# Kernel optimization log

Measured on AMD Instinct MI355X. Metric: run time of the kernel, lower is better.

## Reference

```python
import jax, jax.numpy as jnp
import numpy as np

K = 3          # kernel_size
STRIDE = 1
PAD = 1
DIL = 1


def conv2d(x, w, b, stride=STRIDE, pad=PAD, dil=DIL):
    y = jax.lax.conv_general_dilated(
        x, w, window_strides=(stride, stride),
        padding=((pad, pad), (pad, pad)), rhs_dilation=(dil, dil),
        dimension_numbers=('NCHW', 'OIHW', 'NCHW'))
    if b is not None:
        y = y + b[None, :, None, None]
    return y


def bilinear_gather(x, py, px):
    """Zero-padded bilinear sampling.
    x: [B,C,H,W]; py,px: [B,K2,Ho,Wo] float coords. Returns [B,C,K2,Ho,Wo].
    Matches torchvision deform_conv2d: out-of-range corners contribute zero."""
    B, C, H, W = x.shape
    y0 = jnp.floor(py)
    x0 = jnp.floor(px)
    wy1 = py - y0
    wx1 = px - x0
    wy0 = 1.0 - wy1
    wx0 = 1.0 - wx1
    xf = x.reshape(B, C, H * W)

    def corner(yi, xi, wgt):
        valid = (yi >= 0) & (yi < H) & (xi >= 0) & (xi < W)
        yc = jnp.clip(yi, 0, H - 1).astype(jnp.int32)
        xc = jnp.clip(xi, 0, W - 1).astype(jnp.int32)
        idx = (yc * W + xc).reshape(B, 1, -1)            # [B,1,K2*Ho*Wo]
        v = jnp.take_along_axis(xf, idx, axis=2)         # [B,C,K2*Ho*Wo]
        v = v.reshape(B, C, *yi.shape[1:])               # [B,C,K2,Ho,Wo]
        w = (wgt * valid.astype(x.dtype))[:, None]       # [B,1,K2,Ho,Wo]
        return v * w

    return (corner(y0, x0, wy0 * wx0) + corner(y0, x0 + 1, wy0 * wx1)
            + corner(y0 + 1, x0, wy1 * wx0) + corner(y0 + 1, x0 + 1, wy1 * wx1))


def reference(x, w_offset, b_offset, w_mask, b_mask, w_deform):
    B, C, H, W = x.shape
    K2 = K * K
    offset = conv2d(x, w_offset, b_offset)               # [B,2*K2,Ho,Wo]
    mask = jax.nn.sigmoid(conv2d(x, w_mask, b_mask))     # [B,K2,Ho,Wo]
    Ho, Wo = offset.shape[2], offset.shape[3]

    off = offset.reshape(B, K2, 2, Ho, Wo)
    dy, dx = off[:, :, 0], off[:, :, 1]                  # [B,K2,Ho,Wo]

    ky = (jnp.arange(K2) // K).astype(x.dtype) * DIL     # kernel tap row offsets
    kx = (jnp.arange(K2) % K).astype(x.dtype) * DIL
    base_y = (jnp.arange(Ho) * STRIDE - PAD).astype(x.dtype)
    base_x = (jnp.arange(Wo) * STRIDE - PAD).astype(x.dtype)
    py = dy + base_y[None, None, :, None] + ky[None, :, None, None]
    px = dx + base_x[None, None, None, :] + kx[None, :, None, None]

    val = bilinear_gather(x, py, px)                     # [B,C,K2,Ho,Wo]
    val = val * mask[:, None]                            # modulation

    w = w_deform.reshape(w_deform.shape[0], C, K2)       # [Cout,Cin,K2]
    return jnp.einsum('bckhw,ock->bohw', val, w)


def setup_inputs() -> dict:
    key = jax.random.key(0)
    k = jax.random.split(key, 6)
    B, Cin, Cout, H, W = 2, 64, 64, 224, 224
    x = jax.random.normal(k[0], (B, Cin, H, W), dtype=jnp.float32)
    # source zero-inits offset/mask convs; use small random weights to exercise
    # fractional, scattered sampling coordinates.
    w_offset = jax.random.normal(k[1], (2 * K * K, Cin, K, K), dtype=jnp.float32) * 0.01
    b_offset = jnp.zeros((2 * K * K,), dtype=jnp.float32)
    w_mask = jax.random.normal(k[2], (K * K, Cin, K, K), dtype=jnp.float32) * 0.01
    b_mask = jnp.zeros((K * K,), dtype=jnp.float32)
    w_deform = jax.random.normal(k[3], (Cout, Cin, K, K), dtype=jnp.float32) * (1.0 / np.sqrt(Cin * K * K))
    return {"x": x, "w_offset": w_offset, "b_offset": b_offset,
            "w_mask": w_mask, "b_mask": b_mask, "w_deform": w_deform}
```

## Files before the change

kernel.cpp:

```cpp
#include <hip/hip_runtime.h>
#include <hip/hip_bf16.h>
#include <math.h>

constexpr int B    = 2;
constexpr int C    = 64;
constexpr int H    = 224;
constexpr int W    = 224;
constexpr int Hp   = 226;
constexpr int Wp   = 226;
constexpr int OCO  = 18;
constexpr int OM   = 27;
constexpr int COUT = 64;
constexpr int HW   = H * W;
constexpr int NPIX = B * HW;
constexpr int CK   = C * 9;
constexpr int CPB  = 32;

constexpr int PAD_BLKS = (HW / 32) * B;
constexpr int BOR_N    = B * 900 * 8;
constexpr int BOR_BLKS = (BOR_N + 255) / 256;
constexpr int WA_BLKS  = (COUT * CK) / 256;
constexpr int WOM_BLKS = (32 * CK) / 256;

typedef short  bf16x8 __attribute__((ext_vector_type(8)));
typedef float  f32x4  __attribute__((ext_vector_type(4)));

__device__ inline unsigned short f2bf(float f) {
    union { float f; unsigned u; } v; v.f = f;
    unsigned r = v.u + 0x7FFF + ((v.u >> 16) & 1);
    return (unsigned short)(r >> 16);
}
__device__ inline unsigned cvtpk(float a, float b) {
    __hip_bfloat162 h = __float22bfloat162_rn(make_float2(a, b));
    union { __hip_bfloat162 h; unsigned u; } cv; cv.h = h;
    return cv.u;
}
__device__ inline float blo(unsigned u) { union { unsigned u; float f; } c; c.u = u << 16; return c.f; }
__device__ inline float bhi(unsigned u) { union { unsigned u; float f; } c; c.u = u & 0xFFFF0000u; return c.f; }

__global__ __launch_bounds__(256) void k_prep(const float* __restrict__ x,
                                              unsigned short* __restrict__ xp,
                                              const float* __restrict__ wd,
                                              unsigned short* __restrict__ wA,
                                              const float* __restrict__ w_off,
                                              const float* __restrict__ w_msk,
                                              const float* __restrict__ b_off,
                                              const float* __restrict__ b_msk,
                                              unsigned short* __restrict__ womA,
                                              float* __restrict__ biasv) {
    __shared__ float tile[64][33];
    const int bx  = blockIdx.x;
    const int tid = threadIdx.x;

    if (bx < PAD_BLKS) {
        const int b   = bx / (HW / 32);
        const int hw0 = (bx % (HW / 32)) * 32;
        const float* xb = x + (size_t)b * C * HW;
        {
            const int c  = tid >> 2;
            const int hq = (tid & 3) * 8;
            const float* src = xb + (size_t)c * HW + hw0 + hq;
            const float4 a0 = *reinterpret_cast<const float4*>(src);
            const float4 a1 = *reinterpret_cast<const float4*>(src + 4);
            tile[c][hq + 0] = a0.x; tile[c][hq + 1] = a0.y;
            tile[c][hq + 2] = a0.z; tile[c][hq + 3] = a0.w;
            tile[c][hq + 4] = a1.x; tile[c][hq + 5] = a1.y;
            tile[c][hq + 6] = a1.z; tile[c][hq + 7] = a1.w;
        }
        __syncthreads();
        unsigned short* xpb = xp + (size_t)b * Hp * Wp * C;
        const int l15 = tid & 15, hh = tid >> 4;
        const int c = l15 * 4;
#pragma unroll
        for (int half = 0; half < 2; ++half) {
            int hw = hw0 + half * 16 + hh;
            int y = hw / W, xx = hw % W;
            float t0 = tile[c][half * 16 + hh],     t1 = tile[c + 1][half * 16 + hh];
            float t2 = tile[c + 2][half * 16 + hh], t3 = tile[c + 3][half * 16 + hh];
            *reinterpret_cast<uint2*>(xpb + ((size_t)(y + 1) * Wp + (xx + 1)) * C + c) =
                make_uint2(cvtpk(t0, t1), cvtpk(t2, t3));
        }
        return;
    }
    if (bx < PAD_BLKS + BOR_BLKS) {
        int i = (bx - PAD_BLKS) * 256 + tid;
        if (i >= BOR_N) return;
        int chunk = i & 7;
        int cell  = (i >> 3) % 900;
        int b     = (i >> 3) / 900;
        int y, xx;
        if      (cell < 226) { y = 0;              xx = cell; }
        else if (cell < 452) { y = Hp - 1;         xx = cell - 226; }
        else if (cell < 676) { y = cell - 452 + 1; xx = 0; }
        else                 { y = cell - 676 + 1; xx = Wp - 1; }
        uint4 z = make_uint4(0u, 0u, 0u, 0u);
        *reinterpret_cast<uint4*>(xp + ((size_t)b * Hp * Wp + y * Wp + xx) * C + chunk * 8) = z;
        return;
    }
    if (bx < PAD_BLKS + BOR_BLKS + WA_BLKS) {
        int i  = (bx - PAD_BLKS - BOR_BLKS) * 256 + tid;
        int o  = i / CK;
        int kc = i % CK;
        int k  = kc >> 6;
        int c  = kc & 63;
        wA[i] = f2bf(wd[((size_t)o * C + c) * 9 + k]);
        return;
    }
    {
        int i = (bx - PAD_BLKS - BOR_BLKS - WA_BLKS) * 256 + tid;
        if (i < 32) biasv[i] = (i < OCO) ? b_off[i] : (i < OM) ? b_msk[i - OCO] : 0.f;
        int oc = i / CK;
        int kc = i % CK;
        int k  = kc >> 6;
        int c  = kc & 63;
        float v = (oc < OCO) ? w_off[((size_t)oc * C + c) * 9 + k]
                : (oc < OM)  ? w_msk[((size_t)(oc - OCO) * C + c) * 9 + k]
                             : 0.f;
        womA[i] = f2bf(v);
    }
}

__global__ __launch_bounds__(256, 4) void k_fused(const unsigned short* __restrict__ xp,
                                                  const unsigned short* __restrict__ womA,
                                                  const unsigned short* __restrict__ wA,
                                                  const float* __restrict__ biasv,
                                                  float* __restrict__ out) {
    __shared__ __align__(16) unsigned short imcol[CPB * CK];
    __shared__ float som[CPB][28];
    const int tid  = threadIdx.x;
    const int lane = tid & 63;
    const int wv   = tid >> 6;
    const int q    = lane >> 4;
    const int l15  = lane & 15;
    int bid = blockIdx.x;
    bid = (bid & 7) * (gridDim.x >> 3) + (bid >> 3);
    const int pix0 = bid * CPB;
    const int bb   = pix0 / HW;
    const unsigned short* xb = xp + (size_t)bb * Hp * Wp * C;

    const int c0 = l15 * 4;

#pragma unroll
    for (int pi = 0; pi < 2; ++pi) {
        const int p_local = pi * 16 + wv * 4 + q;
        const int pix = pix0 + p_local;
        const int hw  = pix - bb * HW;
        const int y   = hw / W;
        const int xx  = hw % W;
        int wbase = p_local * (CK * 2) + l15 * 8;
        wbase ^= (p_local & 7) << 4;
#pragma unroll
        for (int k = 0; k < 9; ++k) {
            const int ky = k / 3, kx = k % 3;
            const uint2 v = *reinterpret_cast<const uint2*>(
                xb + ((size_t)(y + ky) * Wp + (xx + kx)) * C + c0);
            *reinterpret_cast<uint2*>(reinterpret_cast<char*>(imcol) + wbase + k * 128) = v;
        }
    }
    __syncthreads();

    {
        f32x4 acc = {0.f, 0.f, 0.f, 0.f};
        const int m = wv & 1, n = wv >> 1;
        const unsigned short* a0 = womA + (size_t)(m * 16 + l15) * CK;
        const int row = n * 16 + l15;
#pragma unroll 3
        for (int ks = 0; ks < 18; ++ks) {
            int byte = row * (CK * 2) + ks * 64 + q * 16;
            byte ^= (row & 7) << 4;
            const bf16x8 bfv = *reinterpret_cast<const bf16x8*>(
                reinterpret_cast<const char*>(imcol) + byte);
            const bf16x8 af = *reinterpret_cast<const bf16x8*>(a0 + ks * 32 + q * 8);
            acc = __builtin_amdgcn_mfma_f32_16x16x32_bf16(af, bfv, acc, 0, 0, 0);
        }
        const int pp = n * 16 + l15;
#pragma unroll
        for (int r = 0; r < 4; ++r) {
            const int oc = m * 16 + q * 4 + r;
            if (oc < OM) {
                float v = acc[r] + biasv[oc];
                som[pp][oc] = (oc < OCO) ? v : 1.0f / (1.0f + __expf(-v));
            }
        }
    }
    __syncthreads();

#pragma unroll
    for (int pi = 0; pi < 2; ++pi) {
        const int p_local = pi * 16 + wv * 4 + q;
        const int pix = pix0 + p_local;
        const int hw  = pix - bb * HW;
        const int ho  = hw / W;
        const int wo  = hw - ho * W;
        int wbase = p_local * (CK * 2) + l15 * 8;
        wbase ^= (p_local & 7) << 4;

        int4   po[9];
        float4 pw[9];
#pragma unroll
        for (int k = 0; k < 9; ++k) {
            const int ky = k / 3, kx = k - (k / 3) * 3;
            const float dy = som[p_local][2 * k];
            const float dx = som[p_local][2 * k + 1];
            const float mm = som[p_local][OCO + k];
            const float py = dy + (float)(ho + ky - 1);
            const float px = dx + (float)(wo + kx - 1);
            const float fy = floorf(py), fx = floorf(px);
            const int   y0 = (int)fy,   x0 = (int)fx;
            const float wy1 = py - fy,  wx1 = px - fx;
            const float wy0 = 1.f - wy1, wx0 = 1.f - wx1;
            const bool iy0 = (y0 >= 0) & (y0 < H);
            const bool iy1 = (y0 + 1 >= 0) & (y0 + 1 < H);
            const bool ix0 = (x0 >= 0) & (x0 < W);
            const bool ix1 = (x0 + 1 >= 0) & (x0 + 1 < W);
            const int ya = min(max(y0 + 1, 0), Hp - 1);
            const int yb = min(max(y0 + 2, 0), Hp - 1);
            const int xa = min(max(x0 + 1, 0), Wp - 1);
            const int xc = min(max(x0 + 2, 0), Wp - 1);
            const int rA = ya * Wp, rB = yb * Wp;
            po[k] = make_int4((rA + xa) * C, (rA + xc) * C,
                              (rB + xa) * C, (rB + xc) * C);
            pw[k] = make_float4(
                wy0 * wx0 * mm * ((iy0 & ix0) ? 1.f : 0.f),
                wy0 * wx1 * mm * ((iy0 & ix1) ? 1.f : 0.f),
                wy1 * wx0 * mm * ((iy1 & ix0) ? 1.f : 0.f),
                wy1 * wx1 * mm * ((iy1 & ix1) ? 1.f : 0.f));
        }

        uint2 u00[9], u01[9], u10[9], u11[9];
#pragma unroll
        for (int k = 0; k < 9; ++k) {
            u00[k] = *reinterpret_cast<const uint2*>(xb + po[k].x + c0);
            u01[k] = *reinterpret_cast<const uint2*>(xb + po[k].y + c0);
            u10[k] = *reinterpret_cast<const uint2*>(xb + po[k].z + c0);
            u11[k] = *reinterpret_cast<const uint2*>(xb + po[k].w + c0);
        }
#pragma unroll
        for (int k = 0; k < 9; ++k) {
            const float4 wt = pw[k];
            const float s0 = wt.x * blo(u00[k].x) + wt.y * blo(u01[k].x) + wt.z * blo(u10[k].x) + wt.w * blo(u11[k].x);
            const float s1 = wt.x * bhi(u00[k].x) + wt.y * bhi(u01[k].x) + wt.z * bhi(u10[k].x) + wt.w * bhi(u11[k].x);
            const float s2 = wt.x * blo(u00[k].y) + wt.y * blo(u01[k].y) + wt.z * blo(u10[k].y) + wt.w * blo(u11[k].y);
            const float s3 = wt.x * bhi(u00[k].y) + wt.y * bhi(u01[k].y) + wt.z * bhi(u10[k].y) + wt.w * bhi(u11[k].y);
            *reinterpret_cast<uint2*>(reinterpret_cast<char*>(imcol) + wbase + k * 128) =
                make_uint2(cvtpk(s0, s1), cvtpk(s2, s3));
        }
    }
    __syncthreads();

    f32x4 acc[2] = {{0.f,0.f,0.f,0.f},{0.f,0.f,0.f,0.f}};
    const unsigned short* wrow = wA + (size_t)(wv * 16 + l15) * CK;
#pragma unroll 3
    for (int ks = 0; ks < 18; ++ks) {
        const bf16x8 af = *reinterpret_cast<const bf16x8*>(wrow + ks * 32 + q * 8);
#pragma unroll
        for (int nt = 0; nt < 2; ++nt) {
            const int row = nt * 16 + l15;
            int byte = row * (CK * 2) + ks * 64 + q * 16;
            byte ^= (row & 7) << 4;
            const bf16x8 bfv = *reinterpret_cast<const bf16x8*>(
                reinterpret_cast<const char*>(imcol) + byte);
            acc[nt] = __builtin_amdgcn_mfma_f32_16x16x32_bf16(af, bfv, acc[nt], 0, 0, 0);
        }
    }

    const int o0 = wv * 16 + q * 4;
#pragma unroll
    for (int nt = 0; nt < 2; ++nt) {
        const int pixn = pix0 + nt * 16 + l15;
        const int hw   = pixn - bb * HW;
#pragma unroll
        for (int r = 0; r < 4; ++r)
            out[((size_t)bb * COUT + o0 + r) * HW + hw] = acc[nt][r];
    }
}

extern "C" void kernel_launch(void* const* d_in, const int* in_sizes, int n_in,
                              void* d_out, int out_size, void* d_ws, size_t ws_size,
                              hipStream_t stream) {
    const float* x     = (const float*)d_in[0];
    const float* w_off = (const float*)d_in[1];
    const float* b_off = (const float*)d_in[2];
    const float* w_msk = (const float*)d_in[3];
    const float* b_msk = (const float*)d_in[4];
    const float* w_def = (const float*)d_in[5];
    float* out = (float*)d_out;

    unsigned short* xpadT = (unsigned short*)d_ws;
    float* biasv = (float*)(xpadT + (size_t)B * Hp * Wp * C);
    unsigned short* wA   = (unsigned short*)(biasv + 32);
    unsigned short* womA = wA + (size_t)COUT * CK;

    k_prep<<<PAD_BLKS + BOR_BLKS + WA_BLKS + WOM_BLKS, 256, 0, stream>>>(
        x, xpadT, w_def, wA, w_off, w_msk, b_off, b_msk, womA, biasv);
    k_fused<<<NPIX / CPB, 256, 0, stream>>>(xpadT, womA, wA, biasv, out);
}
```

Measured before the change: 186.5 us.

## Feed offset/mask MFMA directly from global memory and stream bilinear gather per tap

The offset/mask conv no longer stages an im2col tile in LDS. Each wave loads its MFMA B operands straight from the padded NHWC input in global memory, which drops one LDS write/read pass and one barrier. The bilinear sampling loop is also restructured to compute weights, gather and blend per tap, with partial unrolling instead of fully unrolled arrays. This should cut register pressure but exposes less memory-level parallelism, and the direct global loads are redundant across the two M-waves that share a pixel tile.

```diff
diff --git a/kernel.cpp b/kernel.cpp
--- a/kernel.cpp
+++ b/kernel.cpp
@@ -125,7 +125,7 @@
                                                   const unsigned short* __restrict__ wA,
                                                   const float* __restrict__ biasv,
                                                   float* __restrict__ out) {
-    __shared__ __align__(16) unsigned short imcol[CPB * CK];
+    __shared__ __align__(16) unsigned short valT[CPB * CK];
     __shared__ float som[CPB][28];
     const int tid  = threadIdx.x;
     const int lane = tid & 63;
@@ -140,38 +140,25 @@
 
     const int c0 = l15 * 4;
 
-#pragma unroll
-    for (int pi = 0; pi < 2; ++pi) {
-        const int p_local = pi * 16 + wv * 4 + q;
+    {
+        f32x4 acc = {0.f, 0.f, 0.f, 0.f};
+        const int m = wv & 1, n = wv >> 1;
+        const unsigned short* a0 = womA + (size_t)(m * 16 + l15) * CK;
+        const int p_local = n * 16 + l15;
         const int pix = pix0 + p_local;
         const int hw  = pix - bb * HW;
         const int y   = hw / W;
         const int xx  = hw % W;
-        int wbase = p_local * (CK * 2) + l15 * 8;
-        wbase ^= (p_local & 7) << 4;
-#pragma unroll
+#pragma unroll 3
         for (int k = 0; k < 9; ++k) {
-            const int ky = k / 3, kx = k % 3;
-            const uint2 v = *reinterpret_cast<const uint2*>(
-                xb + ((size_t)(y + ky) * Wp + (xx + kx)) * C + c0);
-            *reinterpret_cast<uint2*>(reinterpret_cast<char*>(imcol) + wbase + k * 128) = v;
-        }
-    }
-    __syncthreads();
-
-    {
-        f32x4 acc = {0.f, 0.f, 0.f, 0.f};
-        const int m = wv & 1, n = wv >> 1;
-        const unsigned short* a0 = womA + (size_t)(m * 16 + l15) * CK;
-        const int row = n * 16 + l15;
-#pragma unroll 3
-        for (int ks = 0; ks < 18; ++ks) {
-            int byte = row * (CK * 2) + ks * 64 + q * 16;
-            byte ^= (row & 7) << 4;
-            const bf16x8 bfv = *reinterpret_cast<const bf16x8*>(
-                reinterpret_cast<const char*>(imcol) + byte);
-            const bf16x8 af = *reinterpret_cast<const bf16x8*>(a0 + ks * 32 + q * 8);
-            acc = __builtin_amdgcn_mfma_f32_16x16x32_bf16(af, bfv, acc, 0, 0, 0);
+            const int ky = k / 3, kx = k - (k / 3) * 3;
+            const unsigned short* base = xb + ((size_t)(y + ky) * Wp + (xx + kx)) * C;
+            const bf16x8 b0 = *reinterpret_cast<const bf16x8*>(base + q * 8);
+            const bf16x8 b1 = *reinterpret_cast<const bf16x8*>(base + 32 + q * 8);
+            const bf16x8 af0 = *reinterpret_cast<const bf16x8*>(a0 + (2 * k) * 32 + q * 8);
+            const bf16x8 af1 = *reinterpret_cast<const bf16x8*>(a0 + (2 * k + 1) * 32 + q * 8);
+            acc = __builtin_amdgcn_mfma_f32_16x16x32_bf16(af0, b0, acc, 0, 0, 0);
+            acc = __builtin_amdgcn_mfma_f32_16x16x32_bf16(af1, b1, acc, 0, 0, 0);
         }
         const int pp = n * 16 + l15;
 #pragma unroll
@@ -194,10 +181,7 @@
         const int wo  = hw - ho * W;
         int wbase = p_local * (CK * 2) + l15 * 8;
         wbase ^= (p_local & 7) << 4;
-
-        int4   po[9];
-        float4 pw[9];
-#pragma unroll
+#pragma unroll 3
         for (int k = 0; k < 9; ++k) {
             const int ky = k / 3, kx = k - (k / 3) * 3;
             const float dy = som[p_local][2 * k];
@@ -218,31 +202,19 @@
             const int xa = min(max(x0 + 1, 0), Wp - 1);
             const int xc = min(max(x0 + 2, 0), Wp - 1);
             const int rA = ya * Wp, rB = yb * Wp;
-            po[k] = make_int4((rA + xa) * C, (rA + xc) * C,
-                              (rB + xa) * C, (rB + xc) * C);
-            pw[k] = make_float4(
-                wy0 * wx0 * mm * ((iy0 & ix0) ? 1.f : 0.f),
-                wy0 * wx1 * mm * ((iy0 & ix1) ? 1.f : 0.f),
-                wy1 * wx0 * mm * ((iy1 & ix0) ? 1.f : 0.f),
-                wy1 * wx1 * mm * ((iy1 & ix1) ? 1.f : 0.f));
-        }
-
-        uint2 u00[9], u01[9], u10[9], u11[9];
-#pragma unroll
-        for (int k = 0; k < 9; ++k) {
-            u00[k] = *reinterpret_cast<const uint2*>(xb + po[k].x + c0);
-            u01[k] = *reinterpret_cast<const uint2*>(xb + po[k].y + c0);
-            u10[k] = *reinterpret_cast<const uint2*>(xb + po[k].z + c0);
-            u11[k] = *reinterpret_cast<const uint2*>(xb + po[k].w + c0);
-        }
-#pragma unroll
-        for (int k = 0; k < 9; ++k) {
-            const float4 wt = pw[k];
-            const float s0 = wt.x * blo(u00[k].x) + wt.y * blo(u01[k].x) + wt.z * blo(u10[k].x) + wt.w * blo(u11[k].x);
-            const float s1 = wt.x * bhi(u00[k].x) + wt.y * bhi(u01[k].x) + wt.z * bhi(u10[k].x) + wt.w * bhi(u11[k].x);
-            const float s2 = wt.x * blo(u00[k].y) + wt.y * blo(u01[k].y) + wt.z * blo(u10[k].y) + wt.w * blo(u11[k].y);
-            const float s3 = wt.x * bhi(u00[k].y) + wt.y * bhi(u01[k].y) + wt.z * bhi(u10[k].y) + wt.w * bhi(u11[k].y);
-            *reinterpret_cast<uint2*>(reinterpret_cast<char*>(imcol) + wbase + k * 128) =
+            const float w00 = wy0 * wx0 * mm * ((iy0 & ix0) ? 1.f : 0.f);
+            const float w01 = wy0 * wx1 * mm * ((iy0 & ix1) ? 1.f : 0.f);
+            const float w10 = wy1 * wx0 * mm * ((iy1 & ix0) ? 1.f : 0.f);
+            const float w11 = wy1 * wx1 * mm * ((iy1 & ix1) ? 1.f : 0.f);
+            const uint2 u00 = *reinterpret_cast<const uint2*>(xb + (rA + xa) * C + c0);
+            const uint2 u01 = *reinterpret_cast<const uint2*>(xb + (rA + xc) * C + c0);
+            const uint2 u10 = *reinterpret_cast<const uint2*>(xb + (rB + xa) * C + c0);
+            const uint2 u11 = *reinterpret_cast<const uint2*>(xb + (rB + xc) * C + c0);
+            const float s0 = w00 * blo(u00.x) + w01 * blo(u01.x) + w10 * blo(u10.x) + w11 * blo(u11.x);
+            const float s1 = w00 * bhi(u00.x) + w01 * bhi(u01.x) + w10 * bhi(u10.x) + w11 * bhi(u11.x);
+            const float s2 = w00 * blo(u00.y) + w01 * blo(u01.y) + w10 * blo(u10.y) + w11 * blo(u11.y);
+            const float s3 = w00 * bhi(u00.y) + w01 * bhi(u01.y) + w10 * bhi(u10.y) + w11 * bhi(u11.y);
+            *reinterpret_cast<uint2*>(reinterpret_cast<char*>(valT) + wbase + k * 128) =
                 make_uint2(cvtpk(s0, s1), cvtpk(s2, s3));
         }
     }
@@ -259,7 +231,7 @@
             int byte = row * (CK * 2) + ks * 64 + q * 16;
             byte ^= (row & 7) << 4;
             const bf16x8 bfv = *reinterpret_cast<const bf16x8*>(
-                reinterpret_cast<const char*>(imcol) + byte);
+                reinterpret_cast<const char*>(valT) + byte);
             acc[nt] = __builtin_amdgcn_mfma_f32_16x16x32_bf16(af, bfv, acc[nt], 0, 0, 0);
         }
     }
```

New measurement: 195.5 us. 4.8% more time.
